# Performance work log

Hardware: AMD Instinct MI355X
Metric: run time of the kernel (lower is better)

The kernel has to match this reference:

```python
import jax, jax.numpy as jnp
import numpy as np

TEMPERATURE = 0.07
EPS = 1e-9


def setup_inputs() -> dict:
    key = jax.random.key(0)
    k1, k2, k3 = jax.random.split(key, 3)
    N, D = 8192, 64
    return {
        "query_embeddings": jax.random.normal(k1, (N, D), dtype=jnp.float32),
        "key_embeddings": jax.random.normal(k2, (N, D), dtype=jnp.float32),
        "positive_indices": jax.random.randint(k3, (N,), 0, N),
    }


def _uhg_distances(q, k):
    # Projective (Minkowski signature +...+ -) hyperbolic distance, vectorized cdist-style.
    # inner(a,b) = sum(a_spatial * b_spatial) - a_time * b_time  (last coord is timelike)
    inner_qk = jnp.einsum('nd,md->nm', q[:, :-1], k[:, :-1]) - jnp.outer(q[:, -1], k[:, -1])
    inner_qq = jnp.sum(q[:, :-1] * q[:, :-1], axis=-1) - q[:, -1] * q[:, -1]  # [N]
    inner_kk = jnp.sum(k[:, :-1] * k[:, :-1], axis=-1) - k[:, -1] * k[:, -1]  # [M]
    denom = jnp.sqrt(jnp.maximum(jnp.abs(inner_qq[:, None] * inner_kk[None, :]), EPS))
    ratio = jnp.maximum(jnp.abs(inner_qk) / denom, 1.0 + EPS)
    return jnp.arccosh(ratio)  # [N, M]


def reference(query_embeddings, key_embeddings, positive_indices):
    N = query_embeddings.shape[0]
    distances = _uhg_distances(query_embeddings, key_embeddings)      # [N, N]
    similarities = -distances / TEMPERATURE                           # [N, N]
    # Faithful vectorization of the per-row loop:
    #   logits_i = sims[i] - sims[i, pos_i];  loss_i = -logits_i[0] + logsumexp(logits_i)
    pos_sim = jnp.take_along_axis(similarities, positive_indices[:, None], axis=1)  # [N,1]
    logits = similarities - pos_sim                                   # [N, N]
    per_row = -logits[:, 0] + jax.scipy.special.logsumexp(logits, axis=1)
    infonce_loss = jnp.sum(per_row) / N
    return infonce_loss, similarities, distances
```

## Files before the change

kernel.cpp:

```cpp
#include <hip/hip_runtime.h>
#include <hip/hip_bf16.h>
#include <math.h>


#define NN 8192
#define DD 64

static constexpr float EPSV      = 1e-9f;
static constexpr float NEG_INV_T = -1.0f / 0.07f;

__global__ __launch_bounds__(256) void uhg_transpose_negate(
    const float* __restrict__ K, float* __restrict__ Kt)
{
    __shared__ float T[64][65];
    const int tid = threadIdx.x;
    const int j0  = blockIdx.x * 64;
    {
        const int j = tid >> 2;
        const int c = (tid & 3) * 16;
        const float* src = K + (size_t)(j0 + j) * DD + c;
        #pragma unroll
        for (int u = 0; u < 4; ++u) {
            const float4 v = *reinterpret_cast<const float4*>(src + 4 * u);
            T[j][c + 4*u + 0] = v.x;
            T[j][c + 4*u + 1] = v.y;
            T[j][c + 4*u + 2] = v.z;
            T[j][c + 4*u + 3] = v.w;
        }
    }
    __syncthreads();
    {
        const int d = tid >> 2;
        const int c = (tid & 3) * 16;
        const float sgn = (d == 63) ? -1.0f : 1.0f;
        float* dst = Kt + (size_t)d * NN + j0 + c;
        #pragma unroll
        for (int u = 0; u < 4; ++u) {
            float4 v;
            v.x = sgn * T[c + 4*u + 0][d];
            v.y = sgn * T[c + 4*u + 1][d];
            v.z = sgn * T[c + 4*u + 2][d];
            v.w = sgn * T[c + 4*u + 3][d];
            *reinterpret_cast<float4*>(dst + 4 * u) = v;
        }
    }
}

__global__ __launch_bounds__(256) void uhg_qqkk(
    const float* __restrict__ Q, const float* __restrict__ K,
    float* __restrict__ qq, float* __restrict__ kk)
{
    const int i = blockIdx.x * 256 + threadIdx.x;
    const bool isQ = (i < NN);
    const int r = isQ ? i : (i - NN);
    const float* src = (isQ ? Q : K) + (size_t)r * DD;
    float acc = 0.0f;
    #pragma unroll
    for (int c = 0; c < 15; ++c) {
        const float4 v = *reinterpret_cast<const float4*>(src + 4 * c);
        acc += v.x*v.x + v.y*v.y + v.z*v.z + v.w*v.w;
    }
    const float4 v = *reinterpret_cast<const float4*>(src + 60);
    acc += v.x*v.x + v.y*v.y + v.z*v.z;
    acc -= v.w*v.w;
    (isQ ? qq : kk)[r] = acc;
}

__global__ __launch_bounds__(256) void uhg_main(
    const float* __restrict__ Q, const float* __restrict__ Kt,
    const float* __restrict__ qq, const float* __restrict__ kk,
    float* __restrict__ out_sims, float* __restrict__ out_dist,
    float* __restrict__ Spart, float* __restrict__ sim0part)
{
    constexpr int TM = 32;
    constexpr int CB = 1024;
    constexpr int TN = 256;

    __shared__ float Qs[DD][36];

    const int tid   = threadIdx.x;
    const int tx    = tid & 63;
    const int ty    = tid >> 6;
    const int cs    = blockIdx.x & 7;
    const int row0  = (blockIdx.x >> 3) * TM;
    const int cbase = cs * CB;
    const int wrow  = 8 * ty;

    {
        const int r  = tid >> 3;
        const int dc = (tid & 7) * 8;
        const float* src = Q + (size_t)(row0 + r) * DD + dc;
        const float4 v0 = *reinterpret_cast<const float4*>(src);
        const float4 v1 = *reinterpret_cast<const float4*>(src + 4);
        Qs[dc + 0][r] = v0.x;  Qs[dc + 1][r] = v0.y;
        Qs[dc + 2][r] = v0.z;  Qs[dc + 3][r] = v0.w;
        Qs[dc + 4][r] = v1.x;  Qs[dc + 5][r] = v1.y;
        Qs[dc + 6][r] = v1.z;  Qs[dc + 7][r] = v1.w;
    }

    float rq[8];
    {
        const float4 a = *reinterpret_cast<const float4*>(qq + row0 + wrow);
        const float4 b = *reinterpret_cast<const float4*>(qq + row0 + wrow + 4);
        rq[0]=a.x; rq[1]=a.y; rq[2]=a.z; rq[3]=a.w;
        rq[4]=b.x; rq[5]=b.y; rq[6]=b.z; rq[7]=b.w;
    }

    float s[8]     = {0,0,0,0,0,0,0,0};
    float sim0r[8] = {0,0,0,0,0,0,0,0};

    __syncthreads();

    for (int t = 0; t < CB / TN; ++t) {
        const int c0 = cbase + t * TN;
        const float* kp = Kt + c0 + tx;
        float acc[8][4] = {};

        #pragma unroll 8
        for (int d = 0; d < DD; ++d) {
            const float4 qv0 = *reinterpret_cast<const float4*>(&Qs[d][wrow]);
            const float4 qv1 = *reinterpret_cast<const float4*>(&Qs[d][wrow + 4]);
            const float qa[8] = {qv0.x, qv0.y, qv0.z, qv0.w,
                                 qv1.x, qv1.y, qv1.z, qv1.w};
            const size_t off = (size_t)d * NN;
            float kv[4];
            kv[0] = kp[off];
            kv[1] = kp[off + 64];
            kv[2] = kp[off + 128];
            kv[3] = kp[off + 192];
            #pragma unroll
            for (int rr = 0; rr < 8; ++rr)
                #pragma unroll
                for (int i = 0; i < 4; ++i)
                    acc[rr][i] = fmaf(qa[rr], kv[i], acc[rr][i]);
        }

        float rk[4];
        rk[0] = kk[c0 + tx];
        rk[1] = kk[c0 + tx + 64];
        rk[2] = kk[c0 + tx + 128];
        rk[3] = kk[c0 + tx + 192];

        #pragma unroll
        for (int rr = 0; rr < 8; ++rr) {
            const size_t rowoff = (size_t)(row0 + wrow + rr) * NN + c0 + tx;
            float* psr = out_sims + rowoff;
            float* pdr = out_dist + rowoff;
            #pragma unroll
            for (int i = 0; i < 4; ++i) {
                const float inner = acc[rr][i];
                const float dd2 = fmaxf(fabsf(rq[rr] * rk[i]), EPSV);
                float dist = 0.0f, sim = 0.0f, e = 1.0f;
                if (inner * inner > dd2 * 0.9999f) {
                    const float ratio = fmaxf(fabsf(inner) / sqrtf(dd2), 1.0f);
                    dist = __logf(ratio + sqrtf(fmaf(ratio, ratio, -1.0f)));
                    sim  = dist * NEG_INV_T;
                    e    = __expf(sim);
                }
                __builtin_nontemporal_store(dist, pdr + 64 * i);
                __builtin_nontemporal_store(sim,  psr + 64 * i);
                if (cs == 0 && t == 0 && i == 0 && tx == 0) sim0r[rr] = sim;
                s[rr] += e;
            }
        }
    }

    #pragma unroll
    for (int rr = 0; rr < 8; ++rr) {
        float v = s[rr];
        #pragma unroll
        for (int mask = 32; mask > 0; mask >>= 1)
            v += __shfl_xor(v, mask, 64);
        s[rr] = v;
    }
    if (tx == 0) {
        #pragma unroll
        for (int rr = 0; rr < 8; ++rr) {
            const int row = row0 + wrow + rr;
            Spart[cs * NN + row] = s[rr];
            if (cs == 0) sim0part[row] = sim0r[rr];
        }
    }
}

__global__ __launch_bounds__(256) void uhg_finalize(
    const float* __restrict__ Spart, const float* __restrict__ sim0part,
    float* __restrict__ out)
{
    __shared__ float red[256];
    const int tid = threadIdx.x;
    float a = 0.0f;
    for (int r = tid; r < NN; r += 256) {
        float S = 0.0f;
        #pragma unroll
        for (int q = 0; q < 8; ++q) S += Spart[q * NN + r];
        a += -sim0part[r] + logf(S);
    }
    red[tid] = a;
    __syncthreads();
    for (int off = 128; off > 0; off >>= 1) {
        if (tid < off) red[tid] += red[tid + off];
        __syncthreads();
    }
    if (tid == 0) out[0] = red[0] / (float)NN;
}

extern "C" void kernel_launch(void* const* d_in, const int* in_sizes, int n_in,
                              void* d_out, int out_size, void* d_ws, size_t ws_size,
                              hipStream_t stream)
{
    const float* Q = (const float*)d_in[0];
    const float* K = (const float*)d_in[1];

    float* out      = (float*)d_out;
    float* out_sims = out + 1;
    float* out_dist = out + 1 + (size_t)NN * NN;

    float* w        = (float*)d_ws;
    float* Kt       = w;
    float* qq       = w + 524288;
    float* kk       = w + 532480;
    float* Spart    = w + 540672;
    float* sim0part = w + 606208;

    uhg_transpose_negate<<<NN / 64, 256, 0, stream>>>(K, Kt);
    uhg_qqkk<<<2 * NN / 256, 256, 0, stream>>>(Q, K, qq, kk);
    uhg_main<<<2048, 256, 0, stream>>>(Q, Kt, qq, kk, out_sims, out_dist,
                                       Spart, sim0part);
    uhg_finalize<<<1, 256, 0, stream>>>(Spart, sim0part, out);
}
```

Measured before the change: 700.7 us.

## Transpose Q globally, widen per-thread tile to 8x8, drop shared-memory staging

Q is now transposed into workspace along with K, so the main kernel reads Q rows as wave-uniform vector loads from global memory instead of staging them through shared memory with a barrier. Each thread now computes an 8x8 register tile over 512 columns in a single pass, using 16 column slices per row group instead of 8, and the launch grows to 4096 blocks. The positive-logit partial is dropped and finalize reads sims[r,0] straight from the output. This removes the LDS traffic and sync and raises FMA reuse per load, at the cost of more registers, possibly lower occupancy, and an extra transpose pass.

```diff
diff --git a/kernel.cpp b/kernel.cpp
--- a/kernel.cpp
+++ b/kernel.cpp
@@ -9,16 +9,20 @@
 static constexpr float EPSV      = 1e-9f;
 static constexpr float NEG_INV_T = -1.0f / 0.07f;
 
-__global__ __launch_bounds__(256) void uhg_transpose_negate(
-    const float* __restrict__ K, float* __restrict__ Kt)
+__global__ __launch_bounds__(256) void uhg_transpose(
+    const float* __restrict__ Q, const float* __restrict__ K,
+    float* __restrict__ Qt, float* __restrict__ Kt)
 {
     __shared__ float T[64][65];
     const int tid = threadIdx.x;
-    const int j0  = blockIdx.x * 64;
+    const bool isK = blockIdx.x < (NN / 64);
+    const int j0  = (isK ? blockIdx.x : blockIdx.x - NN / 64) * 64;
+    const float* src0 = isK ? K : Q;
+    float* dst0 = isK ? Kt : Qt;
     {
         const int j = tid >> 2;
         const int c = (tid & 3) * 16;
-        const float* src = K + (size_t)(j0 + j) * DD + c;
+        const float* src = src0 + (size_t)(j0 + j) * DD + c;
         #pragma unroll
         for (int u = 0; u < 4; ++u) {
             const float4 v = *reinterpret_cast<const float4*>(src + 4 * u);
@@ -32,8 +36,8 @@
     {
         const int d = tid >> 2;
         const int c = (tid & 3) * 16;
-        const float sgn = (d == 63) ? -1.0f : 1.0f;
-        float* dst = Kt + (size_t)d * NN + j0 + c;
+        const float sgn = (isK && d == 63) ? -1.0f : 1.0f;
+        float* dst = dst0 + (size_t)d * NN + j0 + c;
         #pragma unroll
         for (int u = 0; u < 4; ++u) {
             float4 v;
@@ -67,102 +71,75 @@
 }
 
 __global__ __launch_bounds__(256) void uhg_main(
-    const float* __restrict__ Q, const float* __restrict__ Kt,
+    const float* __restrict__ Qt, const float* __restrict__ Kt,
     const float* __restrict__ qq, const float* __restrict__ kk,
     float* __restrict__ out_sims, float* __restrict__ out_dist,
-    float* __restrict__ Spart, float* __restrict__ sim0part)
-{
-    constexpr int TM = 32;
-    constexpr int CB = 1024;
-    constexpr int TN = 256;
-
-    __shared__ float Qs[DD][36];
-
+    float* __restrict__ Spart)
+{
     const int tid   = threadIdx.x;
     const int tx    = tid & 63;
     const int ty    = tid >> 6;
-    const int cs    = blockIdx.x & 7;
-    const int row0  = (blockIdx.x >> 3) * TM;
-    const int cbase = cs * CB;
-    const int wrow  = 8 * ty;
-
-    {
-        const int r  = tid >> 3;
-        const int dc = (tid & 7) * 8;
-        const float* src = Q + (size_t)(row0 + r) * DD + dc;
-        const float4 v0 = *reinterpret_cast<const float4*>(src);
-        const float4 v1 = *reinterpret_cast<const float4*>(src + 4);
-        Qs[dc + 0][r] = v0.x;  Qs[dc + 1][r] = v0.y;
-        Qs[dc + 2][r] = v0.z;  Qs[dc + 3][r] = v0.w;
-        Qs[dc + 4][r] = v1.x;  Qs[dc + 5][r] = v1.y;
-        Qs[dc + 6][r] = v1.z;  Qs[dc + 7][r] = v1.w;
+    const int slice = blockIdx.x & 15;
+    const int row0  = (blockIdx.x >> 4) * 32;
+    const int c0    = slice * 512;
+    const int wrow  = __builtin_amdgcn_readfirstlane(row0 + 8 * ty);
+
+    const float* qp = Qt + wrow;
+    const float* kp = Kt + c0 + tx;
+
+    float acc[8][8] = {};
+
+    #pragma unroll 4
+    for (int d = 0; d < DD; ++d) {
+        const size_t off = (size_t)d * NN;
+        const float4 qv0 = *reinterpret_cast<const float4*>(qp + off);
+        const float4 qv1 = *reinterpret_cast<const float4*>(qp + off + 4);
+        const float qa[8] = {qv0.x, qv0.y, qv0.z, qv0.w,
+                             qv1.x, qv1.y, qv1.z, qv1.w};
+        float kv[8];
+        #pragma unroll
+        for (int i = 0; i < 8; ++i) kv[i] = kp[off + 64 * i];
+        #pragma unroll
+        for (int rr = 0; rr < 8; ++rr)
+            #pragma unroll
+            for (int i = 0; i < 8; ++i)
+                acc[rr][i] = fmaf(qa[rr], kv[i], acc[rr][i]);
     }
 
     float rq[8];
     {
-        const float4 a = *reinterpret_cast<const float4*>(qq + row0 + wrow);
-        const float4 b = *reinterpret_cast<const float4*>(qq + row0 + wrow + 4);
+        const float4 a = *reinterpret_cast<const float4*>(qq + wrow);
+        const float4 b = *reinterpret_cast<const float4*>(qq + wrow + 4);
         rq[0]=a.x; rq[1]=a.y; rq[2]=a.z; rq[3]=a.w;
         rq[4]=b.x; rq[5]=b.y; rq[6]=b.z; rq[7]=b.w;
     }
-
-    float s[8]     = {0,0,0,0,0,0,0,0};
-    float sim0r[8] = {0,0,0,0,0,0,0,0};
-
-    __syncthreads();
-
-    for (int t = 0; t < CB / TN; ++t) {
-        const int c0 = cbase + t * TN;
-        const float* kp = Kt + c0 + tx;
-        float acc[8][4] = {};
-
-        #pragma unroll 8
-        for (int d = 0; d < DD; ++d) {
-            const float4 qv0 = *reinterpret_cast<const float4*>(&Qs[d][wrow]);
-            const float4 qv1 = *reinterpret_cast<const float4*>(&Qs[d][wrow + 4]);
-            const float qa[8] = {qv0.x, qv0.y, qv0.z, qv0.w,
-                                 qv1.x, qv1.y, qv1.z, qv1.w};
-            const size_t off = (size_t)d * NN;
-            float kv[4];
-            kv[0] = kp[off];
-            kv[1] = kp[off + 64];
-            kv[2] = kp[off + 128];
-            kv[3] = kp[off + 192];
-            #pragma unroll
-            for (int rr = 0; rr < 8; ++rr)
-                #pragma unroll
-                for (int i = 0; i < 4; ++i)
-                    acc[rr][i] = fmaf(qa[rr], kv[i], acc[rr][i]);
+    float rk[8];
+    #pragma unroll
+    for (int i = 0; i < 8; ++i) rk[i] = kk[c0 + tx + 64 * i];
+
+    float s[8];
+    #pragma unroll
+    for (int rr = 0; rr < 8; ++rr) {
+        const size_t rowoff = (size_t)(wrow + rr) * NN + c0 + tx;
+        float* psr = out_sims + rowoff;
+        float* pdr = out_dist + rowoff;
+        float sr = 0.0f;
+        #pragma unroll
+        for (int i = 0; i < 8; ++i) {
+            const float inner = acc[rr][i];
+            const float dd2 = fmaxf(fabsf(rq[rr] * rk[i]), EPSV);
+            float dist = 0.0f, sim = 0.0f, e = 1.0f;
+            if (inner * inner > dd2 * 0.9999f) {
+                const float ratio = fmaxf(fabsf(inner) / sqrtf(dd2), 1.0f);
+                dist = __logf(ratio + sqrtf(fmaf(ratio, ratio, -1.0f)));
+                sim  = dist * NEG_INV_T;
+                e    = __expf(sim);
+            }
+            __builtin_nontemporal_store(dist, pdr + 64 * i);
+            __builtin_nontemporal_store(sim,  psr + 64 * i);
+            sr += e;
         }
-
-        float rk[4];
-        rk[0] = kk[c0 + tx];
-        rk[1] = kk[c0 + tx + 64];
-        rk[2] = kk[c0 + tx + 128];
-        rk[3] = kk[c0 + tx + 192];
-
-        #pragma unroll
-        for (int rr = 0; rr < 8; ++rr) {
-            const size_t rowoff = (size_t)(row0 + wrow + rr) * NN + c0 + tx;
-            float* psr = out_sims + rowoff;
-            float* pdr = out_dist + rowoff;
-            #pragma unroll
-            for (int i = 0; i < 4; ++i) {
-                const float inner = acc[rr][i];
-                const float dd2 = fmaxf(fabsf(rq[rr] * rk[i]), EPSV);
-                float dist = 0.0f, sim = 0.0f, e = 1.0f;
-                if (inner * inner > dd2 * 0.9999f) {
-                    const float ratio = fmaxf(fabsf(inner) / sqrtf(dd2), 1.0f);
-                    dist = __logf(ratio + sqrtf(fmaf(ratio, ratio, -1.0f)));
-                    sim  = dist * NEG_INV_T;
-                    e    = __expf(sim);
-                }
-                __builtin_nontemporal_store(dist, pdr + 64 * i);
-                __builtin_nontemporal_store(sim,  psr + 64 * i);
-                if (cs == 0 && t == 0 && i == 0 && tx == 0) sim0r[rr] = sim;
-                s[rr] += e;
-            }
-        }
+        s[rr] = sr;
     }
 
     #pragma unroll
@@ -175,16 +152,13 @@
     }
     if (tx == 0) {
         #pragma unroll
-        for (int rr = 0; rr < 8; ++rr) {
-            const int row = row0 + wrow + rr;
-            Spart[cs * NN + row] = s[rr];
-            if (cs == 0) sim0part[row] = sim0r[rr];
-        }
+        for (int rr = 0; rr < 8; ++rr)
+            Spart[(size_t)slice * NN + wrow + rr] = s[rr];
     }
 }
 
 __global__ __launch_bounds__(256) void uhg_finalize(
-    const float* __restrict__ Spart, const float* __restrict__ sim0part,
+    const float* __restrict__ Spart, const float* __restrict__ out_sims,
     float* __restrict__ out)
 {
     __shared__ float red[256];
@@ -193,8 +167,8 @@
     for (int r = tid; r < NN; r += 256) {
         float S = 0.0f;
         #pragma unroll
-        for (int q = 0; q < 8; ++q) S += Spart[q * NN + r];
-        a += -sim0part[r] + logf(S);
+        for (int q = 0; q < 16; ++q) S += Spart[(size_t)q * NN + r];
+        a += -out_sims[(size_t)r * NN] + logf(S);
     }
     red[tid] = a;
     __syncthreads();
@@ -216,16 +190,16 @@
     float* out_sims = out + 1;
     float* out_dist = out + 1 + (size_t)NN * NN;
 
-    float* w        = (float*)d_ws;
-    float* Kt       = w;
-    float* qq       = w + 524288;
-    float* kk       = w + 532480;
-    float* Spart    = w + 540672;
-    float* sim0part = w + 606208;
-
-    uhg_transpose_negate<<<NN / 64, 256, 0, stream>>>(K, Kt);
+    float* w     = (float*)d_ws;
+    float* Kt    = w;
+    float* Qt    = w + 524288;
+    float* qq    = w + 1048576;
+    float* kk    = w + 1056768;
+    float* Spart = w + 1064960;
+
+    uhg_transpose<<<2 * NN / 64, 256, 0, stream>>>(Q, K, Qt, Kt);
     uhg_qqkk<<<2 * NN / 256, 256, 0, stream>>>(Q, K, qq, kk);
-    uhg_main<<<2048, 256, 0, stream>>>(Q, Kt, qq, kk, out_sims, out_dist,
-                                       Spart, sim0part);
-    uhg_finalize<<<1, 256, 0, stream>>>(Spart, sim0part, out);
-}
+    uhg_main<<<4096, 256, 0, stream>>>(Qt, Kt, qq, kk, out_sims, out_dist,
+                                       Spart);
+    uhg_finalize<<<1, 256, 0, stream>>>(Spart, out_sims, out);
+}
```

Measured after the change: 695.2 us. About the same (-0.8%).
